# Performance work log

Hardware: AMD Instinct MI355X
Metric: run time of the kernel (lower is better)

## Reference

```python
import jax, jax.numpy as jnp
import numpy as np

EPS = 1e-5
BT_BATCH = 32       # BarlowTwinsLoss init batch_size (divides c)
BT_LAMBD = 0.005

def seg_sum(v, idx, n):
    return jax.ops.segment_sum(v, idx, num_segments=n)

def seg_mean(v, idx, n):
    s = seg_sum(v, idx, n)
    c = seg_sum(jnp.ones((v.shape[0],), v.dtype), idx, n)
    return s / jnp.maximum(c, 1.0)[:, None]

def gcn_conv(x, W, b, edge_index):
    n = x.shape[0]
    src, dst = edge_index[0], edge_index[1]
    xw = x @ W
    deg = 1.0 + seg_sum(jnp.ones(src.shape, x.dtype), dst, n)  # self-loop included
    norm = jax.lax.rsqrt(deg[src] * deg[dst])
    out = seg_sum(norm[:, None] * xw[src], dst, n) + xw / deg[:, None]
    return out + b

def barlow(z1, z2):
    # z-score with unbiased std (torch.std), then BatchNorm1d(affine=False) stats
    def std1(z):
        return (z - z.mean(0)) / jnp.std(z, axis=0, ddof=1)
    def bn(z):
        return (z - z.mean(0)) / jnp.sqrt(z.var(0) + EPS)
    a, b = bn(std1(z1)), bn(std1(z2))
    c = (a.T @ b) / BT_BATCH
    d = jnp.diagonal(c)
    on_diag = jnp.sum((d - 1.0) ** 2)
    off_diag = jnp.sum(c ** 2) - jnp.sum(d ** 2)
    return on_diag + BT_LAMBD * off_diag

def layernorm(t, g, b):
    m = t.mean(-1, keepdims=True)
    v = t.var(-1, keepdims=True)
    return g * (t - m) / jnp.sqrt(v + EPS) + b

def setup_inputs() -> dict:
    key = jax.random.key(0)
    ks = jax.random.split(key, 24)
    N, M, d, B = 50000, 10000, 128, 32
    NNZ, EG, EE = 200000, 600000, 160000
    s = 1.0 / np.sqrt(d)
    inp = {
        'x': jax.random.normal(ks[0], (N, d), jnp.float32),
        'hyperedge_feature': jax.random.normal(ks[1], (M, d), jnp.float32),
        'node_coord': jax.random.normal(ks[2], (N, 3), jnp.float32),
        'hyperedge_node_idx': jax.random.randint(ks[3], (NNZ,), 0, N),
        'hyperedge_edge_idx': jax.random.randint(ks[4], (NNZ,), 0, M),
        'node_batch_idx': jnp.sort(jax.random.randint(ks[5], (N,), 0, B)),
        'hyperedge_batch_idx': jnp.sort(jax.random.randint(ks[6], (M,), 0, B)),
        'X_X': jax.random.randint(ks[7], (2, EG), 0, N),
        'E_E': jax.random.randint(ks[8], (2, EE), 0, M),
        'num_graphs': B,
        'Wv': jax.random.normal(ks[9], (d, d), jnp.float32) * s,
        'bv': jnp.zeros((d,), jnp.float32),
        'We': jax.random.normal(ks[10], (d, d), jnp.float32) * s,
        'be': jnp.zeros((d,), jnp.float32),
        'Wx': jax.random.normal(ks[11], (d, d), jnp.float32) * s,
        'bx': jnp.zeros((d,), jnp.float32),
        'Weg': jax.random.normal(ks[12], (d, d), jnp.float32) * s,
        'beg': jnp.zeros((d,), jnp.float32),
        'ln_g': jnp.ones((d,), jnp.float32),
        'ln_b': jnp.zeros((d,), jnp.float32),
        'Wf': jax.random.normal(ks[13], (2 * d, d), jnp.float32) * (1.0 / np.sqrt(2 * d)),
        'bf': jnp.zeros((d,), jnp.float32),
    }
    return inp

def reference(x, hyperedge_feature, node_coord, hyperedge_node_idx, hyperedge_edge_idx,
              node_batch_idx, hyperedge_batch_idx, X_X, E_E, num_graphs,
              Wv, bv, We, be, Wx, bx, Weg, beg, ln_g, ln_b, Wf, bf):
    N, d = x.shape
    M = hyperedge_feature.shape[0]
    ni, ei = hyperedge_node_idx, hyperedge_edge_idx
    # E_HypergraphConv: node<->hyperedge bipartite message passing + EGNN-style coord update
    xw = x @ Wv + bv                     # [N, d]
    ew = hyperedge_feature @ We + be     # [M, d]
    e_conv = seg_mean(xw[ni], ei, M)     # hyperedge update from member nodes
    z_conv = seg_mean(ew[ei], ni, N)     # node update from incident hyperedges
    edge_coord = seg_mean(node_coord[ni], ei, M)          # [M, 3]
    rel = node_coord[ni] - edge_coord[ei]                 # [nnz, 3]
    phi = jnp.tanh(jnp.sum(xw[ni] * ew[ei], -1, keepdims=True)
                   * jax.lax.rsqrt(jnp.asarray(float(d), x.dtype)))
    update_coord = node_coord + seg_mean(rel * phi, ni, N)
    # implicit graph branches
    z_imp = gcn_conv(x, Wx, bx, X_X)
    e_imp = gcn_conv(hyperedge_feature, Weg, beg, E_E)
    bt_loss = barlow(z_imp, z_conv) + barlow(e_imp, e_conv)
    # norm -> GELU (erf, torch default) -> dropout(eval=identity) -> residual
    z = jax.nn.gelu(layernorm(z_conv, ln_g, ln_b), approximate=False) + x
    e = jax.nn.gelu(layernorm(e_conv, ln_g, ln_b), approximate=False) + hyperedge_feature
    z_graph = seg_mean(z, node_batch_idx, num_graphs)
    e_graph = seg_mean(e, hyperedge_batch_idx, num_graphs)
    graph = jnp.concatenate([z_graph, e_graph], axis=1) @ Wf + bf
    return z, e, update_coord, graph, bt_loss
```

## Files before the change

### kernel.cpp

```cpp
#include <hip/hip_runtime.h>
#include <hip/hip_bf16.h>

#define NB 32
#define GPN 512
#define GPM 128
#define RGRP 16

__device__ __forceinline__ float wave_sum(float v) {
#pragma unroll
  for (int off = 32; off; off >>= 1) v += __shfl_xor(v, off);
  return v;
}
__device__ __forceinline__ int wave_sum_i(int v) {
#pragma unroll
  for (int off = 32; off; off >>= 1) v += __shfl_xor(v, off);
  return v;
}

__device__ __forceinline__ float bf2f(unsigned short u) {
  return __uint_as_float(((unsigned int)u) << 16);
}
__device__ __forceinline__ unsigned short f2bf(float f) {
  unsigned int v = __float_as_uint(f);
  return (unsigned short)((v + 0x7FFFu + ((v >> 16) & 1u)) >> 16);
}

__device__ __forceinline__ void gemm_body(const float* __restrict__ X,
                                          const float* __restrict__ W1,
                                          const float* __restrict__ b1,
                                          float* __restrict__ out1,
                                          const float* __restrict__ W2,
                                          unsigned short* __restrict__ out2, int rows,
                                          int blk, float (*xs)[132]) {
  const int t = threadIdx.x;
  const int c4 = t & 31;
  const int rg = t >> 5;
  const int r0 = blk * 64;
#pragma unroll
  for (int i = 0; i < 8; i++) {
    const int idx = t + i * 256;
    const int row = idx >> 5, cc = idx & 31;
    const int gr = r0 + row;
    float4 v = make_float4(0.f, 0.f, 0.f, 0.f);
    if (gr < rows) v = ((const float4*)X)[(size_t)gr * 32 + cc];
    *(float4*)&xs[row][cc * 4] = v;
  }
  __syncthreads();
  const float4* W1v = (const float4*)W1;
  const float4* W2v = (const float4*)W2;
  const float4 b4 = ((const float4*)b1)[c4];
  float4 acc1[8], acc2[8];
#pragma unroll
  for (int i = 0; i < 8; i++) {
    acc1[i] = b4;
    acc2[i] = make_float4(0.f, 0.f, 0.f, 0.f);
  }
  const int rbase = rg * 8;
#pragma unroll 2
  for (int k = 0; k < 128; k++) {
    const float4 w1 = W1v[k * 32 + c4];
    const float4 w2 = W2v[k * 32 + c4];
#pragma unroll
    for (int i = 0; i < 8; i++) {
      const float xv = xs[rbase + i][k];
      acc1[i].x = fmaf(xv, w1.x, acc1[i].x);
      acc1[i].y = fmaf(xv, w1.y, acc1[i].y);
      acc1[i].z = fmaf(xv, w1.z, acc1[i].z);
      acc1[i].w = fmaf(xv, w1.w, acc1[i].w);
      acc2[i].x = fmaf(xv, w2.x, acc2[i].x);
      acc2[i].y = fmaf(xv, w2.y, acc2[i].y);
      acc2[i].z = fmaf(xv, w2.z, acc2[i].z);
      acc2[i].w = fmaf(xv, w2.w, acc2[i].w);
    }
  }
#pragma unroll
  for (int i = 0; i < 8; i++) {
    const int gr = r0 + rbase + i;
    if (gr < rows) {
      ((float4*)out1)[(size_t)gr * 32 + c4] = acc1[i];
      ushort4 o;
      o.x = f2bf(acc2[i].x);
      o.y = f2bf(acc2[i].y);
      o.z = f2bf(acc2[i].z);
      o.w = f2bf(acc2[i].w);
      ((ushort4*)out2)[(size_t)gr * 32 + c4] = o;
    }
  }
}

__global__ __launch_bounds__(256) void fused_stage1(
    const float* __restrict__ x, const float* __restrict__ Wv,
    const float* __restrict__ bv, float* __restrict__ xw,
    const float* __restrict__ Wx, unsigned short* __restrict__ xw2, int N, int nbGN,
    const float* __restrict__ hf, const float* __restrict__ We,
    const float* __restrict__ be, float* __restrict__ ew,
    const float* __restrict__ Weg, unsigned short* __restrict__ ew2, int M, int nbGM,
    const int* __restrict__ ni, const int* __restrict__ ei, int nnz,
    const int* __restrict__ xx, int eg, const int* __restrict__ ee, int eeN,
    int* cnt_n, int* cnt_e, int* cnt_gx, int* cnt_ge, int* rank_pn, int* rank_pe,
    int* rank_g, int* rank_h, const float* __restrict__ coord, float* ec) {
  __shared__ float xs[64][132];
  const int b = blockIdx.x;
  if (b < nbGN) {
    gemm_body(x, Wv, bv, xw, Wx, xw2, N, b, xs);
    return;
  }
  if (b < nbGN + nbGM) {
    gemm_body(hf, We, be, ew, Weg, ew2, M, b - nbGN, xs);
    return;
  }
  const int cb = b - nbGN - nbGM;
  int i = cb * 1024 + (int)threadIdx.x;
#pragma unroll
  for (int k = 0; k < 4; k++, i += 256) {
    if (i < nnz) {
      const int n = ni[i], e = ei[i];
      rank_pn[i] = atomicAdd(&cnt_n[n], 1);
      rank_pe[i] = atomicAdd(&cnt_e[e], 1);
      atomicAdd(&ec[e * 3 + 0], coord[n * 3 + 0]);
      atomicAdd(&ec[e * 3 + 1], coord[n * 3 + 1]);
      atomicAdd(&ec[e * 3 + 2], coord[n * 3 + 2]);
    } else if (i < nnz + eg) {
      const int j = i - nnz;
      rank_g[j] = atomicAdd(&cnt_gx[xx[eg + j]], 1);
    } else if (i < nnz + eg + eeN) {
      const int j = i - nnz - eg;
      rank_h[j] = atomicAdd(&cnt_ge[ee[eeN + j]], 1);
    }
  }
}

__global__ __launch_bounds__(256) void scan_partial(
    const int* __restrict__ c0, int n0, const int* __restrict__ c1, int n1,
    const int* __restrict__ c2, int n2, const int* __restrict__ c3, int n3,
    int nb0, int nb1, int nb2, int nb3, int* __restrict__ bsums) {
  const int gb = blockIdx.x;
  const int* cnt;
  int lb, n;
  if (gb < nb0) { cnt = c0; lb = gb; n = n0; }
  else if (gb < nb0 + nb1) { cnt = c1; lb = gb - nb0; n = n1; }
  else if (gb < nb0 + nb1 + nb2) { cnt = c2; lb = gb - nb0 - nb1; n = n2; }
  else { cnt = c3; lb = gb - nb0 - nb1 - nb2; n = n3; }
  const int t = threadIdx.x;
  const int base = lb * 4096 + t * 16;
  int s = 0;
#pragma unroll
  for (int i = 0; i < 16; i++) {
    const int idx = base + i;
    if (idx < n) s += cnt[idx];
  }
  const int wsum = wave_sum_i(s);
  __shared__ int wsm[4];
  if ((t & 63) == 0) wsm[t >> 6] = wsum;
  __syncthreads();
  if (t == 0) bsums[gb] = wsm[0] + wsm[1] + wsm[2] + wsm[3];
}

__global__ void scan_bsums(const int* __restrict__ bsums, int nb0, int nb1, int nb2,
                           int nb3, int* __restrict__ bbase, int* __restrict__ totals) {
  if (threadIdx.x) return;
  int segs[4] = {nb0, nb1, nb2, nb3};
  int gb = 0;
  for (int a = 0; a < 4; a++) {
    int run = 0;
    for (int i = 0; i < segs[a]; i++) {
      bbase[gb] = run;
      run += bsums[gb];
      gb++;
    }
    totals[a] = run;
  }
}

__global__ __launch_bounds__(256) void scan_final(
    int* __restrict__ c0, int* rp0, float* rs0, float* ecd0, int n0,
    int* __restrict__ c1, int* rp1, float* rs1, float* ecd1, int n1,
    int* __restrict__ c2, int* rp2, float* rs2, float* ecd2, int n2,
    int* __restrict__ c3, int* rp3, float* rs3, float* ecd3, int n3,
    int nb0, int nb1, int nb2, int nb3, const int* __restrict__ bbase,
    const int* __restrict__ totals) {
  const int gb = blockIdx.x;
  int* cnt;
  int* rp;
  float* rs;
  float* ecd;
  int lb, n, a;
  if (gb < nb0) { cnt = c0; rp = rp0; rs = rs0; ecd = ecd0; lb = gb; n = n0; a = 0; }
  else if (gb < nb0 + nb1) { cnt = c1; rp = rp1; rs = rs1; ecd = ecd1; lb = gb - nb0; n = n1; a = 1; }
  else if (gb < nb0 + nb1 + nb2) { cnt = c2; rp = rp2; rs = rs2; ecd = ecd2; lb = gb - nb0 - nb1; n = n2; a = 2; }
  else { cnt = c3; rp = rp3; rs = rs3; ecd = ecd3; lb = gb - nb0 - nb1 - nb2; n = n3; a = 3; }
  const int t = threadIdx.x;
  const int base = lb * 4096 + t * 16;
  int vals[16];
  int s = 0;
#pragma unroll
  for (int i = 0; i < 16; i++) {
    const int idx = base + i;
    vals[i] = (idx < n) ? cnt[idx] : 0;
    s += vals[i];
  }
  __shared__ int tsum[256];
  tsum[t] = s;
  __syncthreads();
  for (int off = 1; off < 256; off <<= 1) {
    const int v = (t >= off) ? tsum[t - off] : 0;
    __syncthreads();
    tsum[t] += v;
    __syncthreads();
  }
  int run = bbase[gb] + (t ? tsum[t - 1] : 0);
#pragma unroll
  for (int i = 0; i < 16; i++) {
    const int idx = base + i;
    if (idx < n) {
      rp[idx] = run;
      if (rs) rs[idx] = rsqrtf(1.f + (float)vals[i]);
      if (ecd) {
        const float inv = 1.f / fmaxf((float)vals[i], 1.f);
        ecd[idx * 3 + 0] *= inv;
        ecd[idx * 3 + 1] *= inv;
        ecd[idx * 3 + 2] *= inv;
      }
      run += vals[i];
    }
  }
  if (t == 0 && lb == 0) rp[n] = totals[a];
}

__global__ __launch_bounds__(256) void fused_fill(
    const int* __restrict__ ni, const int* __restrict__ ei, int nnz,
    const int* __restrict__ xx, int eg, const int* __restrict__ ee, int eeN,
    const int* __restrict__ rp_n, const int* __restrict__ rp_e,
    const int* __restrict__ rp_gx, const int* __restrict__ rp_ge,
    const int* __restrict__ rank_pn, const int* __restrict__ rank_pe,
    const int* __restrict__ rank_g, const int* __restrict__ rank_h, int* adj_n,
    int* adj_e, int* adj_gx, int* adj_ge, int nbFill, const int* __restrict__ nbi,
    int n, int* cbn, const int* __restrict__ hbi, int m, int* cbe) {
  const int b = blockIdx.x;
  const int t = threadIdx.x;
  if (b < nbFill) {
    int i = b * 1024 + t;
#pragma unroll
    for (int k = 0; k < 4; k++, i += 256) {
      if (i < nnz) {
        const int n0 = ni[i], e0 = ei[i];
        adj_n[rp_n[n0] + rank_pn[i]] = e0;
        adj_e[rp_e[e0] + rank_pe[i]] = n0;
      } else if (i < nnz + eg) {
        const int j = i - nnz;
        adj_gx[rp_gx[xx[eg + j]] + rank_g[j]] = xx[j];
      } else if (i < nnz + eg + eeN) {
        const int j = i - nnz - eg;
        adj_ge[rp_ge[ee[eeN + j]] + rank_h[j]] = ee[j];
      }
    }
    return;
  }
  const bool B = (b - nbFill) != 0;
  const int* idx = B ? hbi : nbi;
  const int nn = B ? m : n;
  int* out = B ? cbe : cbn;
  const int g = t;
  if (g >= NB) return;
  int lo = 0, hi = nn;
  while (lo < hi) { int mid = (lo + hi) >> 1; if (idx[mid] < g) lo = mid + 1; else hi = mid; }
  const int l = lo;
  lo = 0; hi = nn;
  while (lo < hi) { int mid = (lo + hi) >> 1; if (idx[mid] < g + 1) lo = mid + 1; else hi = mid; }
  out[g] = lo - l;
}

__device__ __forceinline__ void gcn_body(const unsigned short* __restrict__ xw,
                                         const int* __restrict__ rowptr,
                                         const int* __restrict__ adj,
                                         const float* __restrict__ rs,
                                         const float* __restrict__ bias,
                                         float* __restrict__ out, int n, int lb) {
  const int r = (lb * 256 + (int)threadIdx.x) >> 6;
  const int lane = threadIdx.x & 63;
  if (r >= n) return;
  const int lo = rowptr[r], hi = rowptr[r + 1];
  const float rd = rs[r];
  float2 acc = make_float2(0.f, 0.f);
  for (int base = lo; base < hi; base += 64) {
    const int mm = min(64, hi - base);
    int aj = 0;
    float rj = 0.f;
    if (base + lane < hi) {
      aj = adj[base + lane];
      rj = rs[aj];
    }
    for (int j = 0; j < mm; j++) {
      const int s = __shfl(aj, j);
      const float w = __shfl(rj, j);
      const ushort2 u = ((const ushort2*)xw)[(size_t)s * 64 + lane];
      acc.x = fmaf(w, bf2f(u.x), acc.x);
      acc.y = fmaf(w, bf2f(u.y), acc.y);
    }
  }
  const ushort2 su = ((const ushort2*)xw)[(size_t)r * 64 + lane];
  const float2 bb = ((const float2*)bias)[lane];
  float2 o;
  o.x = fmaf(rd, acc.x, fmaf(rd * rd, bf2f(su.x), bb.x));
  o.y = fmaf(rd, acc.y, fmaf(rd * rd, bf2f(su.y), bb.y));
  ((float2*)out)[(size_t)r * 64 + lane] = o;
}

__global__ __launch_bounds__(256) void fused_gathers(
    const float* __restrict__ ew, const float* __restrict__ xw,
    const float* __restrict__ coord, const float* __restrict__ ecoord,
    const int* __restrict__ rp_n, const int* __restrict__ adj_n,
    float* __restrict__ z_conv, float* __restrict__ outc, int N, int nbNode,
    const unsigned short* __restrict__ xw2, const int* __restrict__ rp_gx,
    const int* __restrict__ adj_gx, const float* __restrict__ rs_gx,
    const float* __restrict__ bx, float* __restrict__ outz, int nbGcnN,
    const unsigned short* __restrict__ ew2, const int* __restrict__ rp_ge,
    const int* __restrict__ adj_ge, const float* __restrict__ rs_ge,
    const float* __restrict__ beg, float* __restrict__ oute, int M, int nbGcnM,
    const int* __restrict__ rp_e, const int* __restrict__ adj_e,
    float* __restrict__ e_conv) {
  const int b = blockIdx.x;
  const int t = threadIdx.x;
  const int lane = t & 63;
  if (b < nbNode) {
    const int r = (b * 256 + t) >> 6;
    if (r >= N) return;
    const int lo = rp_n[r], hi = rp_n[r + 1];
    const float2 a = ((const float2*)xw)[(size_t)r * 64 + lane];
    const float myc = (lane < 3) ? coord[r * 3 + lane] : 0.f;
    float2 acc = make_float2(0.f, 0.f);
    float cacc = 0.f;
    for (int base = lo; base < hi; base += 64) {
      const int mm = min(64, hi - base);
      int aj = (base + lane < hi) ? adj_n[base + lane] : 0;
      for (int j = 0; j < mm; j++) {
        const int e = __shfl(aj, j);
        const float2 bb = ((const float2*)ew)[(size_t)e * 64 + lane];
        acc.x += bb.x;
        acc.y += bb.y;
        const float dot = wave_sum(fmaf(a.x, bb.x, a.y * bb.y));
        const float ph = tanhf(dot * 0.08838834764831845f);
        if (lane < 3) cacc = fmaf(myc - ecoord[e * 3 + lane], ph, cacc);
      }
    }
    const float inv = 1.f / fmaxf((float)(hi - lo), 1.f);
    ((float2*)z_conv)[(size_t)r * 64 + lane] = make_float2(acc.x * inv, acc.y * inv);
    if (lane < 3) outc[r * 3 + lane] = myc + cacc * inv;
    return;
  }
  if (b < nbNode + nbGcnN) {
    gcn_body(xw2, rp_gx, adj_gx, rs_gx, bx, outz, N, b - nbNode);
    return;
  }
  if (b < nbNode + nbGcnN + nbGcnM) {
    gcn_body(ew2, rp_ge, adj_ge, rs_ge, beg, oute, M, b - nbNode - nbGcnN);
    return;
  }
  const int lb = b - nbNode - nbGcnN - nbGcnM;
  const int e = (lb * 256 + t) >> 6;
  if (e >= M) return;
  const int lo = rp_e[e], hi = rp_e[e + 1];
  float2 acc = make_float2(0.f, 0.f);
  for (int base = lo; base < hi; base += 64) {
    const int mm = min(64, hi - base);
    int aj = (base + lane < hi) ? adj_e[base + lane] : 0;
    for (int j = 0; j < mm; j++) {
      const int nidx = __shfl(aj, j);
      const float2 v = ((const float2*)xw)[(size_t)nidx * 64 + lane];
      acc.x += v.x;
      acc.y += v.y;
    }
  }
  const float inv = 1.f / fmaxf((float)(hi - lo), 1.f);
  ((float2*)e_conv)[(size_t)e * 64 + lane] = make_float2(acc.x * inv, acc.y * inv);
}

__global__ __launch_bounds__(256) void gram_partial2(
    const float* __restrict__ Z1a, const float* __restrict__ Z2a, int na,
    float* __restrict__ parta, const float* __restrict__ Z1b,
    const float* __restrict__ Z2b, int nbm, float* __restrict__ partb,
    float* __restrict__ st, int nblkA) {
  const bool A = (int)blockIdx.x < nblkA;
  const int pid = A ? blockIdx.x : blockIdx.x - nblkA;
  const float* Z1 = A ? Z1a : Z1b;
  const float* Z2 = A ? Z2a : Z2b;
  const int n = A ? na : nbm;
  const int gparts = A ? GPN : GPM;
  float* part = (A ? parta : partb) + (size_t)pid * 16384;
  float* sum1 = st + (A ? 0 : 512);
  float* ssq1 = sum1 + 128;
  float* sum2 = sum1 + 256;
  float* ssq2 = sum1 + 384;
  __shared__ float4 s1[256], s2[256];
  const int t = threadIdx.x;
  const int ti = t >> 4, tj = t & 15;
  const int rpb = (n + gparts - 1) / gparts;
  const int lo = pid * rpb, hi = min(lo + rpb, n);
  float acc[8][8];
#pragma unroll
  for (int i = 0; i < 8; i++)
#pragma unroll
    for (int j = 0; j < 8; j++) acc[i][j] = 0.f;
  float cs = 0.f, cq = 0.f;
  const float* s1f = (const float*)s1;
  const float* s2f = (const float*)s2;
  const int c = t & 127;
  const bool low = t < 128;
  for (int rb = lo; rb < hi; rb += 8) {
    const int nr = min(8, hi - rb);
    __syncthreads();
    if (t < nr * 32) {
      const int rr = rb + (t >> 5);
      s1[t] = ((const float4*)Z1)[(size_t)rr * 32 + (t & 31)];
      s2[t] = ((const float4*)Z2)[(size_t)rr * 32 + (t & 31)];
    }
    __syncthreads();
    for (int r = 0; r < nr; r++) {
      const float4 a0 = s1[r * 32 + ti * 2], a1 = s1[r * 32 + ti * 2 + 1];
      const float4 b0 = s2[r * 32 + tj * 2], b1 = s2[r * 32 + tj * 2 + 1];
      const float av[8] = {a0.x, a0.y, a0.z, a0.w, a1.x, a1.y, a1.z, a1.w};
      const float bv[8] = {b0.x, b0.y, b0.z, b0.w, b1.x, b1.y, b1.z, b1.w};
#pragma unroll
      for (int i = 0; i < 8; i++)
#pragma unroll
        for (int j = 0; j < 8; j++) acc[i][j] = fmaf(av[i], bv[j], acc[i][j]);
      const float v = low ? s1f[r * 128 + c] : s2f[r * 128 + c];
      cs += v;
      cq = fmaf(v, v, cq);
    }
  }
  float4* P = (float4*)part;
#pragma unroll
  for (int i = 0; i < 8; i++) {
    P[(ti * 8 + i) * 32 + tj * 2] = make_float4(acc[i][0], acc[i][1], acc[i][2], acc[i][3]);
    P[(ti * 8 + i) * 32 + tj * 2 + 1] = make_float4(acc[i][4], acc[i][5], acc[i][6], acc[i][7]);
  }
  if (low) {
    atomicAdd(&sum1[c], cs);
    atomicAdd(&ssq1[c], cq);
  } else {
    atomicAdd(&sum2[c], cs);
    atomicAdd(&ssq2[c], cq);
  }
}

__global__ __launch_bounds__(256) void fused_reduce_ln(
    const float* __restrict__ parta, float* __restrict__ G1,
    const float* __restrict__ partb, float* __restrict__ G2,
    const float* __restrict__ convA, const float* __restrict__ residA,
    float* __restrict__ outA, int nA, int lnA, const float* __restrict__ convB,
    const float* __restrict__ residB, float* __restrict__ outB, int nBm,
    const float* __restrict__ g, const float* __restrict__ bvec) {
  const int b = blockIdx.x;
  const int t = threadIdx.x;
  const int NRED = (GPN / RGRP + GPM / RGRP) * 16;
  if (b < NRED) {
    const int nga = GPN / RGRP;
    const int slice = b & 15;
    const int grp = b >> 4;
    const bool A = grp < nga;
    const float* part = A ? parta : partb;
    float* G = A ? G1 : G2;
    const int g0 = (A ? grp : grp - nga) * RGRP;
    const int e = slice * 1024 + t * 4;
    float4 s = make_float4(0.f, 0.f, 0.f, 0.f);
#pragma unroll 4
    for (int p = 0; p < RGRP; p++) {
      const float4 v = *(const float4*)&part[(size_t)(g0 + p) * 16384 + e];
      s.x += v.x;
      s.y += v.y;
      s.z += v.z;
      s.w += v.w;
    }
    atomicAdd(&G[e], s.x);
    atomicAdd(&G[e + 1], s.y);
    atomicAdd(&G[e + 2], s.z);
    atomicAdd(&G[e + 3], s.w);
    return;
  }
  const int b2 = b - NRED;
  const bool A = b2 < lnA;
  const int lb = A ? b2 : b2 - lnA;
  const float* conv = A ? convA : convB;
  const float* resid = A ? residA : residB;
  float* out = A ? outA : outB;
  const int rows = A ? nA : nBm;
  const int w = (lb * 256 + t) >> 6;
  const int lane = t & 63;
  if (w >= rows) return;
  const float2 v = ((const float2*)conv)[(size_t)w * 64 + lane];
  const float m = wave_sum(v.x + v.y) * (1.f / 128.f);
  const float q = wave_sum(fmaf(v.x, v.x, v.y * v.y)) * (1.f / 128.f);
  const float rstd = rsqrtf(q - m * m + 1e-5f);
  const float2 gg = ((const float2*)g)[lane];
  const float2 bb = ((const float2*)bvec)[lane];
  const float2 rr = ((const float2*)resid)[(size_t)w * 64 + lane];
  float y0 = fmaf(gg.x, (v.x - m) * rstd, bb.x);
  float y1 = fmaf(gg.y, (v.y - m) * rstd, bb.y);
  y0 = 0.5f * y0 * (1.f + erff(y0 * 0.7071067811865476f));
  y1 = 0.5f * y1 * (1.f + erff(y1 * 0.7071067811865476f));
  float2 o;
  o.x = y0 + rr.x;
  o.y = y1 + rr.y;
  ((float2*)out)[(size_t)w * 64 + lane] = o;
}

__global__ __launch_bounds__(256) void fused_fin_pool(
    const float* __restrict__ G1, const float* __restrict__ G2,
    const float* __restrict__ st, float nA, float nB, float* outbt,
    const float* __restrict__ ZA, const int* __restrict__ bidxA, int n, int spA,
    float* poolA, const float* __restrict__ ZB, const int* __restrict__ bidxB, int m,
    float* poolB) {
  __shared__ float s1s[128], m1s[128], s2s[128], m2s[128];
  __shared__ float red[256];
  const int b = blockIdx.x;
  const int t = threadIdx.x;
  if (b < 2) {
    const bool A = b == 0;
    const float* G = A ? G1 : G2;
    const float* sum1 = st + (A ? 0 : 512);
    const float* ssq1 = sum1 + 128;
    const float* sum2 = sum1 + 256;
    const float* ssq2 = sum1 + 384;
    const float nn = A ? nA : nB;
    if (t < 128) {
      const float inv_n = 1.f / nn;
      const float bnf = (nn - 1.f) * inv_n + 1e-5f;
      float mu = sum1[t] * inv_n;
      float vu = (ssq1[t] * inv_n - mu * mu) * nn / (nn - 1.f);
      s1s[t] = rsqrtf(vu * bnf);
      m1s[t] = mu;
      mu = sum2[t] * inv_n;
      vu = (ssq2[t] * inv_n - mu * mu) * nn / (nn - 1.f);
      s2s[t] = rsqrtf(vu * bnf);
      m2s[t] = mu;
    }
    __syncthreads();
    float on = 0.f, off = 0.f;
    for (int idx = t; idx < 16384; idx += 256) {
      const int i = idx >> 7, j = idx & 127;
      const float c = s1s[i] * s2s[j] * (G[idx] - nn * m1s[i] * m2s[j]) * (1.f / 32.f);
      if (i == j) {
        const float dd = c - 1.f;
        on += dd * dd;
      } else {
        off += c * c;
      }
    }
    red[t] = on + 0.005f * off;
    __syncthreads();
    for (int s = 128; s; s >>= 1) {
      if (t < s) red[t] += red[t + s];
      __syncthreads();
    }
    if (t == 0) atomicAdd(outbt, red[0]);
    return;
  }
  const int pb = b - 2;
  const bool A = pb < spA;
  const int lb = A ? pb : pb - spA;
  const float* Z = A ? ZA : ZB;
  const int* bidx = A ? bidxA : bidxB;
  const int n2 = A ? n : m;
  float* pool = A ? poolA : poolB;
  const int c = t & 127;
  const int h = t >> 7;
  const int r0 = lb * 128 + h * 64;
  const int re = min(lb * 128 + (h + 1) * 64, n2);
  if (r0 >= n2) return;
  float acc = 0.f;
  int cur = bidx[r0];
  for (int r = r0; r < re; r++) {
    const int bb = bidx[r];
    if (bb != cur) {
      atomicAdd(&pool[cur * 128 + c], acc);
      acc = 0.f;
      cur = bb;
    }
    acc += Z[(size_t)r * 128 + c];
  }
  atomicAdd(&pool[cur * 128 + c], acc);
}

__global__ __launch_bounds__(128) void graph_gemm(
    const float* __restrict__ zg, const float* __restrict__ eg,
    const int* __restrict__ cnz, const int* __restrict__ cne,
    const float* __restrict__ Wf, const float* __restrict__ bf, float* out) {
  __shared__ float cat[256];
  const int g = blockIdx.x, t = threadIdx.x;
  cat[t] = zg[g * 128 + t] / fmaxf((float)cnz[g], 1.f);
  cat[128 + t] = eg[g * 128 + t] / fmaxf((float)cne[g], 1.f);
  __syncthreads();
  float acc = bf[t];
#pragma unroll 8
  for (int k = 0; k < 256; k++) acc = fmaf(cat[k], Wf[k * 128 + t], acc);
  out[g * 128 + t] = acc;
}

extern "C" void kernel_launch(void* const* d_in, const int* in_sizes, int n_in,
                              void* d_out, int out_size, void* d_ws, size_t ws_size,
                              hipStream_t stream) {
  const float* x = (const float*)d_in[0];
  const float* hf = (const float*)d_in[1];
  const float* coord = (const float*)d_in[2];
  const int* ni = (const int*)d_in[3];
  const int* ei = (const int*)d_in[4];
  const int* nb = (const int*)d_in[5];
  const int* hb = (const int*)d_in[6];
  const int* xx = (const int*)d_in[7];
  const int* ee = (const int*)d_in[8];
  const float* Wv = (const float*)d_in[10];
  const float* bv = (const float*)d_in[11];
  const float* We = (const float*)d_in[12];
  const float* be = (const float*)d_in[13];
  const float* Wx = (const float*)d_in[14];
  const float* bx = (const float*)d_in[15];
  const float* Weg = (const float*)d_in[16];
  const float* beg = (const float*)d_in[17];
  const float* lng = (const float*)d_in[18];
  const float* lnb = (const float*)d_in[19];
  const float* Wf = (const float*)d_in[20];
  const float* bf = (const float*)d_in[21];

  const int N = in_sizes[0] / 128;
  const int M = in_sizes[1] / 128;
  const int NNZ = in_sizes[3];
  const int EG = in_sizes[7] / 2;
  const int EE = in_sizes[8] / 2;

  float* ws = (float*)d_ws;
  size_t o = 0;
  float* xw = ws + o;     o += (size_t)N * 128;
  float* ew = ws + o;     o += (size_t)M * 128;
  unsigned short* xw2 = (unsigned short*)(ws + o); o += (size_t)N * 64;
  unsigned short* ew2 = (unsigned short*)(ws + o); o += (size_t)M * 64;
  float* z_conv = ws + o; o += (size_t)N * 128;
  float* e_conv = ws + o; o += (size_t)M * 128;
  float* rs_gx = ws + o;  o += N;
  float* rs_ge = ws + o;  o += M;
  const size_t fz0 = o;
  float* ecoord = ws + o; o += (size_t)M * 3;
  float* G1 = ws + o;     o += 16384;
  float* G2 = ws + o;     o += 16384;
  float* st = ws + o;     o += 1024;
  float* zg = ws + o;     o += NB * 128;
  float* eg_p = ws + o;   o += NB * 128;
  const size_t fz1 = o;
  int* wsi = (int*)(ws + o);
  size_t oi = 0;
  int* cnt_n = wsi + oi;  oi += N;
  int* cnt_e = wsi + oi;  oi += M;
  int* cnt_gx = wsi + oi; oi += N;
  int* cnt_ge = wsi + oi; oi += M;
  const size_t iz1 = oi;
  int* rp_n = wsi + oi;   oi += N + 1;
  int* rp_e = wsi + oi;   oi += M + 1;
  int* rp_gx = wsi + oi;  oi += N + 1;
  int* rp_ge = wsi + oi;  oi += M + 1;
  int* adj_n = wsi + oi;  oi += NNZ;
  int* adj_e = wsi + oi;  oi += NNZ;
  int* adj_gx = wsi + oi; oi += EG;
  int* adj_ge = wsi + oi; oi += EE;
  int* rank_pn = wsi + oi; oi += NNZ;
  int* rank_pe = wsi + oi; oi += NNZ;
  int* rank_g = wsi + oi;  oi += EG;
  int* rank_h = wsi + oi;  oi += EE;
  int* cbn = wsi + oi;    oi += NB;
  int* cbe = wsi + oi;    oi += NB;
  int* bsums = wsi + oi;  oi += 64;
  int* bbase = wsi + oi;  oi += 64;
  int* totals = wsi + oi; oi += 4;

  float* gpartA = xw;
  float* gpartB = xw + (size_t)GPN * 16384;

  float* outz = (float*)d_out;
  float* oute = outz + (size_t)N * 128;
  float* outc = oute + (size_t)M * 128;
  float* outg = outc + (size_t)N * 3;
  float* outbt = outg + NB * 128;

  hipMemsetAsync(ws + fz0, 0, (fz1 - fz0) * 4, stream);
  hipMemsetAsync(wsi, 0, iz1 * 4, stream);
  hipMemsetAsync(outbt, 0, 4, stream);

  const int nbGN = (N + 63) / 64, nbGM = (M + 63) / 64;
  const int tot = NNZ + EG + EE;
  const int nbCnt = (tot + 1023) >> 10;
  fused_stage1<<<nbGN + nbGM + nbCnt, 256, 0, stream>>>(
      x, Wv, bv, xw, Wx, xw2, N, nbGN, hf, We, be, ew, Weg, ew2, M, nbGM, ni, ei, NNZ,
      xx, EG, ee, EE, cnt_n, cnt_e, cnt_gx, cnt_ge, rank_pn, rank_pe, rank_g, rank_h,
      coord, ecoord);

  const int nb0 = (N + 4095) >> 12, nb1 = (M + 4095) >> 12;
  const int sgrid = 2 * nb0 + 2 * nb1;
  scan_partial<<<sgrid, 256, 0, stream>>>(cnt_n, N, cnt_e, M, cnt_gx, N, cnt_ge, M,
                                          nb0, nb1, nb0, nb1, bsums);
  scan_bsums<<<1, 64, 0, stream>>>(bsums, nb0, nb1, nb0, nb1, bbase, totals);
  scan_final<<<sgrid, 256, 0, stream>>>(
      cnt_n, rp_n, nullptr, nullptr, N, cnt_e, rp_e, nullptr, ecoord, M, cnt_gx,
      rp_gx, rs_gx, nullptr, N, cnt_ge, rp_ge, rs_ge, nullptr, M, nb0, nb1, nb0, nb1,
      bbase, totals);

  const int nbFill = (tot + 1023) >> 10;
  fused_fill<<<nbFill + 2, 256, 0, stream>>>(
      ni, ei, NNZ, xx, EG, ee, EE, rp_n, rp_e, rp_gx, rp_ge, rank_pn, rank_pe, rank_g,
      rank_h, adj_n, adj_e, adj_gx, adj_ge, nbFill, nb, N, cbn, hb, M, cbe);

  const int nbNode = (N + 3) / 4, nbGcnN = (N + 3) / 4, nbGcnM = (M + 3) / 4,
            nbHedge = (M + 3) / 4;
  fused_gathers<<<nbNode + nbGcnN + nbGcnM + nbHedge, 256, 0, stream>>>(
      ew, xw, coord, ecoord, rp_n, adj_n, z_conv, outc, N, nbNode, xw2, rp_gx, adj_gx,
      rs_gx, bx, outz, nbGcnN, ew2, rp_ge, adj_ge, rs_ge, beg, oute, M, nbGcnM, rp_e,
      adj_e, e_conv);

  gram_partial2<<<GPN + GPM, 256, 0, stream>>>(outz, z_conv, N, gpartA, oute, e_conv,
                                               M, gpartB, st, GPN);

  const int lnA = (N + 3) / 4;
  fused_reduce_ln<<<(GPN / RGRP + GPM / RGRP) * 16 + lnA + (M + 3) / 4, 256, 0,
                    stream>>>(gpartA, G1, gpartB, G2, z_conv, x, outz, N, lnA, e_conv,
                              hf, oute, M, lng, lnb);

  const int spA = (N + 127) / 128, spB = (M + 127) / 128;
  fused_fin_pool<<<2 + spA + spB, 256, 0, stream>>>(G1, G2, st, (float)N, (float)M,
                                                    outbt, outz, nb, N, spA, zg, oute,
                                                    hb, M, eg_p);

  graph_gemm<<<NB, 128, 0, stream>>>(zg, eg_p, cbn, cbe, Wf, bf, outg);
}
```

Before: 372.8 us.

## Store xw/ew projections as bf16 and shrink GEMM row tile to 32

The main node and hyperedge projections (xw, ew) are now written in bf16 instead of fp32, and the gather kernels read and convert them, halving the bytes of those heavily gathered arrays. The GEMM row tile drops from 64 to 32 rows per block, giving more blocks and less shared memory and register pressure per block. The workspace is rearranged so that the rank arrays sit in the freed space, and the Barlow partial-sum counts (GPN/GPM) are reduced to fit. Storing in bf16 lowers precision for the means and the tanh coordinate weights.

```diff
diff --git a/kernel.cpp b/kernel.cpp
--- a/kernel.cpp
+++ b/kernel.cpp
@@ -2,8 +2,8 @@
 #include <hip/hip_bf16.h>
 
 #define NB 32
-#define GPN 512
-#define GPM 128
+#define GPN 448
+#define GPM 80
 #define RGRP 16
 
 __device__ __forceinline__ float wave_sum(float v) {
@@ -28,16 +28,16 @@
 __device__ __forceinline__ void gemm_body(const float* __restrict__ X,
                                           const float* __restrict__ W1,
                                           const float* __restrict__ b1,
-                                          float* __restrict__ out1,
+                                          unsigned short* __restrict__ out1,
                                           const float* __restrict__ W2,
                                           unsigned short* __restrict__ out2, int rows,
                                           int blk, float (*xs)[132]) {
   const int t = threadIdx.x;
   const int c4 = t & 31;
   const int rg = t >> 5;
-  const int r0 = blk * 64;
-#pragma unroll
-  for (int i = 0; i < 8; i++) {
+  const int r0 = blk * 32;
+#pragma unroll
+  for (int i = 0; i < 4; i++) {
     const int idx = t + i * 256;
     const int row = idx >> 5, cc = idx & 31;
     const int gr = r0 + row;
@@ -49,19 +49,19 @@
   const float4* W1v = (const float4*)W1;
   const float4* W2v = (const float4*)W2;
   const float4 b4 = ((const float4*)b1)[c4];
-  float4 acc1[8], acc2[8];
-#pragma unroll
-  for (int i = 0; i < 8; i++) {
+  float4 acc1[4], acc2[4];
+#pragma unroll
+  for (int i = 0; i < 4; i++) {
     acc1[i] = b4;
     acc2[i] = make_float4(0.f, 0.f, 0.f, 0.f);
   }
-  const int rbase = rg * 8;
-#pragma unroll 2
+  const int rbase = rg * 4;
+#pragma unroll 4
   for (int k = 0; k < 128; k++) {
     const float4 w1 = W1v[k * 32 + c4];
     const float4 w2 = W2v[k * 32 + c4];
 #pragma unroll
-    for (int i = 0; i < 8; i++) {
+    for (int i = 0; i < 4; i++) {
       const float xv = xs[rbase + i][k];
       acc1[i].x = fmaf(xv, w1.x, acc1[i].x);
       acc1[i].y = fmaf(xv, w1.y, acc1[i].y);
@@ -74,32 +74,32 @@
     }
   }
 #pragma unroll
-  for (int i = 0; i < 8; i++) {
+  for (int i = 0; i < 4; i++) {
     const int gr = r0 + rbase + i;
     if (gr < rows) {
-      ((float4*)out1)[(size_t)gr * 32 + c4] = acc1[i];
-      ushort4 o;
-      o.x = f2bf(acc2[i].x);
-      o.y = f2bf(acc2[i].y);
-      o.z = f2bf(acc2[i].z);
-      o.w = f2bf(acc2[i].w);
-      ((ushort4*)out2)[(size_t)gr * 32 + c4] = o;
+      ushort4 o1, o2;
+      o1.x = f2bf(acc1[i].x); o1.y = f2bf(acc1[i].y);
+      o1.z = f2bf(acc1[i].z); o1.w = f2bf(acc1[i].w);
+      o2.x = f2bf(acc2[i].x); o2.y = f2bf(acc2[i].y);
+      o2.z = f2bf(acc2[i].z); o2.w = f2bf(acc2[i].w);
+      ((ushort4*)out1)[(size_t)gr * 32 + c4] = o1;
+      ((ushort4*)out2)[(size_t)gr * 32 + c4] = o2;
     }
   }
 }
 
 __global__ __launch_bounds__(256) void fused_stage1(
     const float* __restrict__ x, const float* __restrict__ Wv,
-    const float* __restrict__ bv, float* __restrict__ xw,
+    const float* __restrict__ bv, unsigned short* __restrict__ xw,
     const float* __restrict__ Wx, unsigned short* __restrict__ xw2, int N, int nbGN,
     const float* __restrict__ hf, const float* __restrict__ We,
-    const float* __restrict__ be, float* __restrict__ ew,
+    const float* __restrict__ be, unsigned short* __restrict__ ew,
     const float* __restrict__ Weg, unsigned short* __restrict__ ew2, int M, int nbGM,
     const int* __restrict__ ni, const int* __restrict__ ei, int nnz,
     const int* __restrict__ xx, int eg, const int* __restrict__ ee, int eeN,
     int* cnt_n, int* cnt_e, int* cnt_gx, int* cnt_ge, int* rank_pn, int* rank_pe,
     int* rank_g, int* rank_h, const float* __restrict__ coord, float* ec) {
-  __shared__ float xs[64][132];
+  __shared__ float xs[32][132];
   const int b = blockIdx.x;
   if (b < nbGN) {
     gemm_body(x, Wv, bv, xw, Wx, xw2, N, b, xs);
@@ -307,7 +307,7 @@
 }
 
 __global__ __launch_bounds__(256) void fused_gathers(
-    const float* __restrict__ ew, const float* __restrict__ xw,
+    const unsigned short* __restrict__ ew, const unsigned short* __restrict__ xw,
     const float* __restrict__ coord, const float* __restrict__ ecoord,
     const int* __restrict__ rp_n, const int* __restrict__ adj_n,
     float* __restrict__ z_conv, float* __restrict__ outc, int N, int nbNode,
@@ -326,7 +326,8 @@
     const int r = (b * 256 + t) >> 6;
     if (r >= N) return;
     const int lo = rp_n[r], hi = rp_n[r + 1];
-    const float2 a = ((const float2*)xw)[(size_t)r * 64 + lane];
+    const ushort2 au = ((const ushort2*)xw)[(size_t)r * 64 + lane];
+    const float2 a = make_float2(bf2f(au.x), bf2f(au.y));
     const float myc = (lane < 3) ? coord[r * 3 + lane] : 0.f;
     float2 acc = make_float2(0.f, 0.f);
     float cacc = 0.f;
@@ -335,7 +336,8 @@
       int aj = (base + lane < hi) ? adj_n[base + lane] : 0;
       for (int j = 0; j < mm; j++) {
         const int e = __shfl(aj, j);
-        const float2 bb = ((const float2*)ew)[(size_t)e * 64 + lane];
+        const ushort2 bu = ((const ushort2*)ew)[(size_t)e * 64 + lane];
+        const float2 bb = make_float2(bf2f(bu.x), bf2f(bu.y));
         acc.x += bb.x;
         acc.y += bb.y;
         const float dot = wave_sum(fmaf(a.x, bb.x, a.y * bb.y));
@@ -366,9 +368,9 @@
     int aj = (base + lane < hi) ? adj_e[base + lane] : 0;
     for (int j = 0; j < mm; j++) {
       const int nidx = __shfl(aj, j);
-      const float2 v = ((const float2*)xw)[(size_t)nidx * 64 + lane];
-      acc.x += v.x;
-      acc.y += v.y;
+      const ushort2 vu = ((const ushort2*)xw)[(size_t)nidx * 64 + lane];
+      acc.x += bf2f(vu.x);
+      acc.y += bf2f(vu.y);
     }
   }
   const float inv = 1.f / fmaxf((float)(hi - lo), 1.f);
@@ -630,10 +632,14 @@
 
   float* ws = (float*)d_ws;
   size_t o = 0;
-  float* xw = ws + o;     o += (size_t)N * 128;
-  float* ew = ws + o;     o += (size_t)M * 128;
+  unsigned short* xw = (unsigned short*)(ws + o);  o += (size_t)N * 64;
+  unsigned short* ew = (unsigned short*)(ws + o);  o += (size_t)M * 64;
   unsigned short* xw2 = (unsigned short*)(ws + o); o += (size_t)N * 64;
   unsigned short* ew2 = (unsigned short*)(ws + o); o += (size_t)M * 64;
+  int* rank_pn = (int*)(ws + o); o += NNZ;
+  int* rank_pe = (int*)(ws + o); o += NNZ;
+  int* rank_g = (int*)(ws + o);  o += EG;
+  int* rank_h = (int*)(ws + o);  o += EE;
   float* z_conv = ws + o; o += (size_t)N * 128;
   float* e_conv = ws + o; o += (size_t)M * 128;
   float* rs_gx = ws + o;  o += N;
@@ -661,18 +667,14 @@
   int* adj_e = wsi + oi;  oi += NNZ;
   int* adj_gx = wsi + oi; oi += EG;
   int* adj_ge = wsi + oi; oi += EE;
-  int* rank_pn = wsi + oi; oi += NNZ;
-  int* rank_pe = wsi + oi; oi += NNZ;
-  int* rank_g = wsi + oi;  oi += EG;
-  int* rank_h = wsi + oi;  oi += EE;
   int* cbn = wsi + oi;    oi += NB;
   int* cbe = wsi + oi;    oi += NB;
   int* bsums = wsi + oi;  oi += 64;
   int* bbase = wsi + oi;  oi += 64;
   int* totals = wsi + oi; oi += 4;
 
-  float* gpartA = xw;
-  float* gpartB = xw + (size_t)GPN * 16384;
+  float* gpartA = ws;
+  float* gpartB = ws + (size_t)GPN * 16384;
 
   float* outz = (float*)d_out;
   float* oute = outz + (size_t)N * 128;
@@ -684,7 +686,7 @@
   hipMemsetAsync(wsi, 0, iz1 * 4, stream);
   hipMemsetAsync(outbt, 0, 4, stream);
 
-  const int nbGN = (N + 63) / 64, nbGM = (M + 63) / 64;
+  const int nbGN = (N + 31) / 32, nbGM = (M + 31) / 32;
   const int tot = NNZ + EG + EE;
   const int nbCnt = (tot + 1023) >> 10;
   fused_stage1<<<nbGN + nbGM + nbCnt, 256, 0, stream>>>(
```

Result: slower. 414.8 us (+11.3%).
